# Performance work log

Measured on AMD Instinct MI355X. Metric: run time of the kernel, lower is better.

Reference implementation:

```python
import jax, jax.numpy as jnp
import numpy as np

N_QUBITS = 8
N_LAYERS = 3
DIM = 2 ** N_QUBITS  # 256


def _ry(t):
    # t: scalar or [B] -> [2,2] or [B,2,2] complex64
    c = jnp.cos(t / 2).astype(jnp.complex64)
    s = jnp.sin(t / 2).astype(jnp.complex64)
    return jnp.stack([jnp.stack([c, -s], -1), jnp.stack([s, c], -1)], -2)


def _rz(t):
    e = jnp.exp(-0.5j * t.astype(jnp.complex64))
    z = jnp.zeros_like(e)
    return jnp.stack([jnp.stack([e, z], -1), jnp.stack([z, jnp.conj(e)], -1)], -2)


def _rx(t):
    c = jnp.cos(t / 2).astype(jnp.complex64)
    s = (-1j) * jnp.sin(t / 2).astype(jnp.complex64)
    return jnp.stack([jnp.stack([c, s], -1), jnp.stack([s, c], -1)], -2)


def _apply_1q(state, U, wire):
    # state: [B, 256] complex64; U: [2,2] (shared) or [B,2,2] (per-sample)
    B = state.shape[0]
    l = 2 ** wire
    r = 2 ** (N_QUBITS - wire - 1)
    s = state.reshape(B, l, 2, r)
    if U.ndim == 2:
        s = jnp.einsum('ij,bljr->blir', U, s)
    else:
        s = jnp.einsum('bij,bljr->blir', U, s)
    return s.reshape(B, DIM)


def _apply_cnot(state, c_wire):
    # CNOT with control c_wire, target c_wire+1 (adjacent, as in the circuit)
    B = state.shape[0]
    l = 2 ** c_wire
    r = 2 ** (N_QUBITS - c_wire - 2)
    s = state.reshape(B, l, 2, 2, r)  # [B, left, ctrl, tgt, right]
    s = jnp.stack([s[:, :, 0], s[:, :, 1, ::-1]], axis=2)  # flip target where ctrl=1
    return s.reshape(B, DIM)


def _circuit(x, weights):
    B = x.shape[0]
    state = jnp.zeros((B, DIM), jnp.complex64).at[:, 0].set(1.0)
    # angle encoding: RY(x_i*pi) then RZ(x_i*pi) on each wire (per-sample angles)
    for i in range(N_QUBITS):
        ang = x[:, i] * jnp.pi
        state = _apply_1q(state, _ry(ang), i)
        state = _apply_1q(state, _rz(ang), i)
    # variational layers: RX(w), RY(w) per qubit, then CNOT ladder
    idx = 0
    for _ in range(N_LAYERS):
        for q in range(N_QUBITS):
            state = _apply_1q(state, _rx(weights[idx]), q)
            state = _apply_1q(state, _ry(weights[idx + 1]), q)
            idx += 2
        for q in range(N_QUBITS - 1):
            state = _apply_cnot(state, q)
    # <Z_i> = P(bit_i = 0) - P(bit_i = 1)
    p = (jnp.abs(state) ** 2).reshape((B,) + (2,) * N_QUBITS)
    outs = []
    for i in range(N_QUBITS):
        axes = tuple(j + 1 for j in range(N_QUBITS) if j != i)
        m = p.sum(axes)  # [B, 2]
        outs.append(m[:, 0] - m[:, 1])
    return jnp.stack(outs, -1).astype(jnp.float32)  # [B, 8]


def setup_inputs() -> dict:
    key = jax.random.key(0)
    k1, k2 = jax.random.split(key)
    x = jax.random.normal(k1, (16384, 8), dtype=jnp.float32)
    weights = jax.random.normal(k2, (48,), dtype=jnp.float32) * 0.1
    return {"x": x, "weights": weights}


def reference(x, weights):
    return _circuit(x, weights)
```

## Files before the change

### kernel.cpp

```cpp
#include <hip/hip_runtime.h>
#include <math.h>

#define PI_F 3.14159265358979323846f

typedef _Float16 h16x8 __attribute__((ext_vector_type(8)));
typedef float f32x4 __attribute__((ext_vector_type(4)));
typedef unsigned int u32x4 __attribute__((ext_vector_type(4)));

#define APAGE 4112
#define P2STR 146


__device__ __forceinline__ void gpair(float2& a, const float2 p, const int mb,
                                      const float g0x, const float g0y,
                                      const float g1x, const float g1y) {
    const float e0y = mb ? -g0y : g0y;
    const float f1x = mb ? -g1x : g1x;
    const float nx = g0x * a.x - e0y * a.y + f1x * p.x - g1y * p.y;
    const float ny = g0x * a.y + e0y * a.x + f1x * p.y + g1y * p.x;
    a.x = nx; a.y = ny;
}

__device__ __forceinline__ void apply_g(float2 a[4], const int b, const int lane,
                                        const float g0x, const float g0y,
                                        const float g1x, const float g1y) {
    if (b >= 2) {
        const int lb = b - 2;
        const int mb = (lane >> lb) & 1;
#pragma unroll
        for (int j = 0; j < 4; ++j) {
            float2 p;
            p.x = __shfl_xor(a[j].x, 1 << lb, 64);
            p.y = __shfl_xor(a[j].y, 1 << lb, 64);
            gpair(a[j], p, mb, g0x, g0y, g1x, g1y);
        }
    } else if (b == 1) {
        float2 o0 = a[0], o1 = a[1], o2 = a[2], o3 = a[3];
        gpair(a[0], o2, 0, g0x, g0y, g1x, g1y);
        gpair(a[2], o0, 1, g0x, g0y, g1x, g1y);
        gpair(a[1], o3, 0, g0x, g0y, g1x, g1y);
        gpair(a[3], o1, 1, g0x, g0y, g1x, g1y);
    } else {
        float2 o0 = a[0], o1 = a[1], o2 = a[2], o3 = a[3];
        gpair(a[0], o1, 0, g0x, g0y, g1x, g1y);
        gpair(a[1], o0, 1, g0x, g0y, g1x, g1y);
        gpair(a[2], o3, 0, g0x, g0y, g1x, g1y);
        gpair(a[3], o2, 1, g0x, g0y, g1x, g1y);
    }
}

__device__ __forceinline__ void apply_cnot_g(float2 a[4], const int cw, const int lane) {
    if (cw <= 4) {
        const int lt = (6 - cw) - 2;
        const int lc = lt + 1;
        const bool ctrl = ((lane >> lc) & 1) != 0;
#pragma unroll
        for (int j = 0; j < 4; ++j) {
            float px = __shfl_xor(a[j].x, 1 << lt, 64);
            float py = __shfl_xor(a[j].y, 1 << lt, 64);
            a[j].x = ctrl ? px : a[j].x;
            a[j].y = ctrl ? py : a[j].y;
        }
    } else if (cw == 5) {
        const bool ctrl = (lane & 1) != 0;
        float2 t;
        t = a[0]; a[0].x = ctrl ? a[2].x : a[0].x; a[0].y = ctrl ? a[2].y : a[0].y;
        a[2].x = ctrl ? t.x : a[2].x; a[2].y = ctrl ? t.y : a[2].y;
        t = a[1]; a[1].x = ctrl ? a[3].x : a[1].x; a[1].y = ctrl ? a[3].y : a[1].y;
        a[3].x = ctrl ? t.x : a[3].x; a[3].y = ctrl ? t.y : a[3].y;
    } else {
        float2 t = a[2]; a[2] = a[3]; a[3] = t;
    }
}

__device__ __forceinline__ unsigned int packh2(float lo, float hi) {
    unsigned short l = __builtin_bit_cast(unsigned short, (_Float16)lo);
    unsigned short h = __builtin_bit_cast(unsigned short, (_Float16)hi);
    return ((unsigned int)h << 16) | (unsigned int)l;
}

__device__ __forceinline__ float2 cmulf(float2 a, float2 b) {
    return make_float2(a.x * b.x - a.y * b.y, a.x * b.y + a.y * b.x);
}

__device__ __forceinline__ h16x8 negh8(h16x8 v) {
    u32x4 u = __builtin_bit_cast(u32x4, v);
    u ^= (u32x4){0x80008000u, 0x80008000u, 0x80008000u, 0x80008000u};
    return __builtin_bit_cast(h16x8, u);
}

__global__ __launch_bounds__(64) void ubuild_kernel(const float* __restrict__ w,
                                                    unsigned short* __restrict__ ub16) {
    __shared__ float wc[48];
    __shared__ float wsn[48];
    const int tid = threadIdx.x;
    if (tid < 48) {
        float s, c;
        __sincosf(w[tid] * 0.5f, &s, &c);
        wc[tid] = c; wsn[tid] = s;
    }
    __syncthreads();

    const int lane = tid;
    const int n = blockIdx.x;

    float2 e0q[8], e1q[8];
#pragma unroll
    for (int q = 0; q < 8; ++q) {
        const int k = 2 * q;
        const float c0 = wc[k], s0 = wsn[k];
        const float c1 = wc[k + 1], s1 = wsn[k + 1];
        const float2 g0 = make_float2(c1 * c0, s1 * s0);
        const float2 g1 = make_float2(-s1 * c0, -c1 * s0);
        const int nq = (n >> (7 - q)) & 1;
        e0q[q] = nq ? g1 : g0;
        e1q[q] = nq ? make_float2(g0.x, -g0.y)
                    : make_float2(-g1.x, g1.y);
    }

    float2 a[4];
#pragma unroll
    for (int j = 0; j < 4; ++j) {
        const int m = lane * 4 + j;
        const int v = m ^ (m >> 1);
        float2 acc = ((v >> 7) & 1) ? e1q[0] : e0q[0];
#pragma unroll
        for (int q = 1; q < 8; ++q)
            acc = cmulf(acc, ((v >> (7 - q)) & 1) ? e1q[q] : e0q[q]);
        a[j] = acc;
    }

#pragma unroll
    for (int L = 1; L < 3; ++L) {
#pragma unroll
        for (int q = 0; q < 8; ++q) {
            const int k = 2 * (L * 8 + q);
            const float c0 = wc[k], s0 = wsn[k];
            const float c1 = wc[k + 1], s1 = wsn[k + 1];
            const float g0x = c1 * c0, g0y = s1 * s0;
            const float g1x = -s1 * c0, g1y = -c1 * s0;
            apply_g(a, 7 - q, lane, g0x, g0y, g1x, g1y);
        }
#pragma unroll
        for (int cwire = 0; cwire < 7; ++cwire) apply_cnot_g(a, cwire, lane);
    }

    const int base = (n >> 5) * 8192 + (n & 31);
#pragma unroll
    for (int j = 0; j < 4; ++j) {
        const int m = lane * 4 + j;
        ub16[base + m * 32] =
            __builtin_bit_cast(unsigned short, (_Float16)a[j].x);
        ub16[65536 + base + m * 32] =
            __builtin_bit_cast(unsigned short, (_Float16)a[j].y);
    }
}

__device__ __forceinline__ void loadB4(h16x8 bf[4], const char* ub, const size_t boff[4],
                                       const int kk) {
#pragma unroll
    for (int f = 0; f < 4; ++f)
        bf[f] = *(const h16x8*)(ub + (size_t)kk * 16384 + boff[f]);
}

__device__ __forceinline__ void loadA8(h16x8 ar[4], h16x8 ai[4], const char* apc,
                                       const unsigned int aoff, const int kk) {
#pragma unroll
    for (int rt = 0; rt < 4; ++rt)
        ar[rt] = *(const h16x8*)(apc + kk * APAGE + rt * 1024 + aoff);
#pragma unroll
    for (int rt = 0; rt < 4; ++rt)
        ai[rt] = *(const h16x8*)(apc + 8 * APAGE + kk * APAGE + rt * 1024 + aoff);
}

__device__ __forceinline__ void mfma32(f32x4 aR[4][2], f32x4 aI[4][2],
                                       const h16x8 ar[4], const h16x8 ai[4],
                                       const h16x8 bf[4]) {
#pragma unroll
    for (int rt = 0; rt < 4; ++rt) {
        const h16x8 nai = negh8(ai[rt]);
#pragma unroll
        for (int cf = 0; cf < 2; ++cf) {
            aR[rt][cf] = __builtin_amdgcn_mfma_f32_16x16x32_f16(ar[rt], bf[cf],
                                                                aR[rt][cf], 0, 0, 0);
            aR[rt][cf] = __builtin_amdgcn_mfma_f32_16x16x32_f16(nai, bf[2 + cf],
                                                                aR[rt][cf], 0, 0, 0);
            aI[rt][cf] = __builtin_amdgcn_mfma_f32_16x16x32_f16(ai[rt], bf[cf],
                                                                aI[rt][cf], 0, 0, 0);
            aI[rt][cf] = __builtin_amdgcn_mfma_f32_16x16x32_f16(ar[rt], bf[2 + cf],
                                                                aI[rt][cf], 0, 0, 0);
        }
    }
}

__global__ __launch_bounds__(512, 2) void gemm_kernel(const float* __restrict__ x,
                                                      const unsigned short* __restrict__ upack,
                                                      float* __restrict__ out) {
    __shared__ __align__(16) char smem[64 * P2STR * 8];

    const int tid = threadIdx.x;
    const int lane = tid & 63;
    const int wv = tid >> 6;
    const int c15 = lane & 15;
    const int g = lane >> 4;

    const char* ub = (const char*)upack;
    size_t boff[4];
    {
        const int cb0 = wv * 32;
        boff[0] = (size_t)(cb0 + c15) * 64 + g * 16;
        boff[1] = (size_t)(cb0 + 16 + c15) * 64 + g * 16;
        boff[2] = 131072 + boff[0];
        boff[3] = 131072 + boff[1];
    }
    h16x8 b0[4], b1[4], b2[4], b3[4];
    loadB4(b0, ub, boff, 0);
    loadB4(b1, ub, boff, 1);
    loadB4(b2, ub, boff, 2);
    loadB4(b3, ub, boff, 3);

    {
        const int row = tid >> 3;
        const int t8 = tid & 7;
        const int grow = blockIdx.x * 64 + row;

        const float4* xp = (const float4*)(x + grow * 8);
        float4 xa = xp[0], xb = xp[1];
        float ang[8] = {xa.x, xa.y, xa.z, xa.w, xb.x, xb.y, xb.z, xb.w};

        float2 v0[8], v1[8];
#pragma unroll
        for (int i = 0; i < 8; ++i) {
            float s, c;
            __sincosf(ang[i] * (PI_F * 0.5f), &s, &c);
            v0[i] = make_float2(c * c, -c * s);
            v1[i] = make_float2(s * c, s * s);
        }

        float2 pre = (t8 & 4) ? v1[0] : v0[0];
        pre = cmulf(pre, (t8 & 2) ? v1[1] : v0[1]);
        pre = cmulf(pre, (t8 & 1) ? v1[2] : v0[2]);

        const int swz = (row >> 1) & 3;
        char* reb = smem + t8 * APAGE + row * 64;
        char* imb = smem + (8 + t8) * APAGE + row * 64;

#pragma unroll
        for (int b4 = 0; b4 < 2; ++b4) {
            float2 p3 = cmulf(pre, b4 ? v1[3] : v0[3]);
#pragma unroll
            for (int b3 = 0; b3 < 2; ++b3) {
                float2 p4 = cmulf(p3, b3 ? v1[4] : v0[4]);
                u32x4 qre, qim;
#pragma unroll
                for (int b2 = 0; b2 < 2; ++b2) {
                    float2 p5 = cmulf(p4, b2 ? v1[5] : v0[5]);
#pragma unroll
                    for (int b1 = 0; b1 < 2; ++b1) {
                        float2 p6 = cmulf(p5, b1 ? v1[6] : v0[6]);
                        const float2 amp0 = cmulf(p6, v0[7]);
                        const float2 amp1 = cmulf(p6, v1[7]);
                        const int pos = (b2 << 1) | b1;
                        qre[pos] = packh2(amp0.x, amp1.x);
                        qim[pos] = packh2(amp0.y, amp1.y);
                    }
                }
                const int c = (b4 << 1) | b3;
                *(u32x4*)(reb + ((c ^ swz) * 16)) = qre;
                *(u32x4*)(imb + ((c ^ swz) * 16)) = qim;
            }
        }
    }
    __syncthreads();

    const unsigned int aoff = c15 * 64 + ((g ^ ((c15 >> 1) & 3)) * 16);
    const char* apc = (const char*)smem;

    f32x4 aR[4][2], aI[4][2];
#pragma unroll
    for (int rt = 0; rt < 4; ++rt)
#pragma unroll
        for (int cf = 0; cf < 2; ++cf) {
            f32x4 z = {0.f, 0.f, 0.f, 0.f};
            aR[rt][cf] = z; aI[rt][cf] = z;
        }

    h16x8 ar0[4], ai0[4], ar1[4], ai1[4];
    loadA8(ar0, ai0, apc, aoff, 0);

    loadA8(ar1, ai1, apc, aoff, 1);  mfma32(aR, aI, ar0, ai0, b0);  loadB4(b0, ub, boff, 4);
    loadA8(ar0, ai0, apc, aoff, 2);  mfma32(aR, aI, ar1, ai1, b1);  loadB4(b1, ub, boff, 5);
    loadA8(ar1, ai1, apc, aoff, 3);  mfma32(aR, aI, ar0, ai0, b2);  loadB4(b2, ub, boff, 6);
    loadA8(ar0, ai0, apc, aoff, 4);  mfma32(aR, aI, ar1, ai1, b3);  loadB4(b3, ub, boff, 7);
    loadA8(ar1, ai1, apc, aoff, 5);  mfma32(aR, aI, ar0, ai0, b0);
    loadA8(ar0, ai0, apc, aoff, 6);  mfma32(aR, aI, ar1, ai1, b1);
    loadA8(ar1, ai1, apc, aoff, 7);  mfma32(aR, aI, ar0, ai0, b2);
                                     mfma32(aR, aI, ar1, ai1, b3);

    __syncthreads();

    {
        float2* P2 = (float2*)smem;
#pragma unroll
        for (int rt = 0; rt < 4; ++rt) {
#pragma unroll
            for (int r = 0; r < 4; ++r) {
                const float p0 = aR[rt][0][r] * aR[rt][0][r] + aI[rt][0][r] * aI[rt][0][r];
                const float p1 = aR[rt][1][r] * aR[rt][1][r] + aI[rt][1][r] * aI[rt][1][r];
                const int row = rt * 16 + g * 4 + r;
                P2[row * P2STR + wv * 18 + c15] = make_float2(p0, p1);
            }
        }
    }
    __syncthreads();

    {
        const float2* P2 = (const float2*)smem;
        const int row = tid >> 3;
        const int w2 = tid & 7;

        const float4* base = (const float4*)(P2 + row * P2STR + w2 * 18);
        float S[16], D[16];
#pragma unroll
        for (int k = 0; k < 8; ++k) {
            const float4 q = base[k];
            S[2 * k]     = q.x + q.y;  D[2 * k]     = q.x - q.y;
            S[2 * k + 1] = q.z + q.w;  D[2 * k + 1] = q.z - q.w;
        }
        float s2[8], w1p[8];
#pragma unroll
        for (int k = 0; k < 8; ++k) { s2[k] = S[2*k] + S[2*k+1]; w1p[k] = S[2*k] - S[2*k+1]; }
        float s4[4], w2p[4];
#pragma unroll
        for (int k = 0; k < 4; ++k) { s4[k] = s2[2*k] + s2[2*k+1]; w2p[k] = s2[2*k] - s2[2*k+1]; }
        const float s8a = s4[0] + s4[1], s8b = s4[2] + s4[3];
        const float W0 = s8a + s8b;
        const float W8 = s8a - s8b;
        const float W4 = (s4[0] - s4[1]) + (s4[2] - s4[3]);
        const float W2 = w2p[0] + w2p[1] + w2p[2] + w2p[3];
        float W1 = 0.f, Sd = 0.f;
#pragma unroll
        for (int k = 0; k < 8; ++k) { W1 += w1p[k]; Sd += D[2*k] + D[2*k+1]; }

        float zp[8];
        zp[0] = (w2 & 4) ? -W0 : W0;
        zp[1] = (w2 & 2) ? -W0 : W0;
        zp[2] = (w2 & 1) ? -W0 : W0;
        zp[3] = Sd;
        zp[4] = W8;
        zp[5] = W4;
        zp[6] = W2;
        zp[7] = W1;

#pragma unroll
        for (int i = 0; i < 8; ++i) {
            zp[i] += __shfl_xor(zp[i], 1, 64);
            zp[i] += __shfl_xor(zp[i], 2, 64);
            zp[i] += __shfl_xor(zp[i], 4, 64);
        }

        if (w2 == 0) {
            float* po = out + (size_t)(blockIdx.x * 64 + row) * 8;
            *(float4*)po       = make_float4(zp[0], zp[1], zp[2], zp[3]);
            *(float4*)(po + 4) = make_float4(zp[4], zp[5], zp[6], zp[7]);
        }
    }
}

extern "C" void kernel_launch(void* const* d_in, const int* in_sizes, int n_in,
                              void* d_out, int out_size, void* d_ws, size_t ws_size,
                              hipStream_t stream) {
    const float* x = (const float*)d_in[0];
    const float* w = (const float*)d_in[1];
    float* out = (float*)d_out;
    const int B = in_sizes[0] / 8;

    unsigned short* ub16 = (unsigned short*)d_ws;
    ubuild_kernel<<<256, 64, 0, stream>>>(w, ub16);

    gemm_kernel<<<B / 64, 512, 0, stream>>>(x, (const unsigned short*)d_ws, out);
}
```

Before: 20.49 us.

## Halve rows per block to 32 and raise occupancy target

Each block now processes 32 batch rows instead of 64, using 16 threads per row for state preparation, 2 row tiles per wave in the MFMA loop, and half the shared memory. The grid doubles and launch bounds now ask for 8 blocks per CU, aiming for more parallelism and better latency hiding across the 256 CUs. In exchange, each block reloads the full unitary from global/L2 for half the rows, doubling B-matrix traffic per output row. Half the threads also sit idle in the final reduction.

```diff
diff --git a/kernel.cpp b/kernel.cpp
--- a/kernel.cpp
+++ b/kernel.cpp
@@ -7,9 +7,9 @@
 typedef float f32x4 __attribute__((ext_vector_type(4)));
 typedef unsigned int u32x4 __attribute__((ext_vector_type(4)));
 
-#define APAGE 4112
+#define ROWS 32
+#define APAGE 2064
 #define P2STR 146
-
 
 __device__ __forceinline__ void gpair(float2& a, const float2 p, const int mb,
                                       const float g0x, const float g0y,
@@ -163,21 +163,21 @@
         bf[f] = *(const h16x8*)(ub + (size_t)kk * 16384 + boff[f]);
 }
 
-__device__ __forceinline__ void loadA8(h16x8 ar[4], h16x8 ai[4], const char* apc,
-                                       const unsigned int aoff, const int kk) {
-#pragma unroll
-    for (int rt = 0; rt < 4; ++rt)
+__device__ __forceinline__ void loadA4c(h16x8 ar[2], h16x8 ai[2], const char* apc,
+                                        const unsigned int aoff, const int kk) {
+#pragma unroll
+    for (int rt = 0; rt < 2; ++rt)
         ar[rt] = *(const h16x8*)(apc + kk * APAGE + rt * 1024 + aoff);
 #pragma unroll
-    for (int rt = 0; rt < 4; ++rt)
+    for (int rt = 0; rt < 2; ++rt)
         ai[rt] = *(const h16x8*)(apc + 8 * APAGE + kk * APAGE + rt * 1024 + aoff);
 }
 
-__device__ __forceinline__ void mfma32(f32x4 aR[4][2], f32x4 aI[4][2],
-                                       const h16x8 ar[4], const h16x8 ai[4],
-                                       const h16x8 bf[4]) {
-#pragma unroll
-    for (int rt = 0; rt < 4; ++rt) {
+__device__ __forceinline__ void mfma16c(f32x4 aR[2][2], f32x4 aI[2][2],
+                                        const h16x8 ar[2], const h16x8 ai[2],
+                                        const h16x8 bf[4]) {
+#pragma unroll
+    for (int rt = 0; rt < 2; ++rt) {
         const h16x8 nai = negh8(ai[rt]);
 #pragma unroll
         for (int cf = 0; cf < 2; ++cf) {
@@ -193,10 +193,10 @@
     }
 }
 
-__global__ __launch_bounds__(512, 2) void gemm_kernel(const float* __restrict__ x,
+__global__ __launch_bounds__(512, 8) void gemm_kernel(const float* __restrict__ x,
                                                       const unsigned short* __restrict__ upack,
                                                       float* __restrict__ out) {
-    __shared__ __align__(16) char smem[64 * P2STR * 8];
+    __shared__ __align__(16) char smem[ROWS * P2STR * 8];
 
     const int tid = threadIdx.x;
     const int lane = tid & 63;
@@ -220,9 +220,9 @@
     loadB4(b3, ub, boff, 3);
 
     {
-        const int row = tid >> 3;
-        const int t8 = tid & 7;
-        const int grow = blockIdx.x * 64 + row;
+        const int row = tid >> 4;
+        const int t16 = tid & 15;
+        const int grow = blockIdx.x * ROWS + row;
 
         const float4* xp = (const float4*)(x + grow * 8);
         float4 xa = xp[0], xb = xp[1];
@@ -237,72 +237,76 @@
             v1[i] = make_float2(s * c, s * s);
         }
 
-        float2 pre = (t8 & 4) ? v1[0] : v0[0];
-        pre = cmulf(pre, (t8 & 2) ? v1[1] : v0[1]);
-        pre = cmulf(pre, (t8 & 1) ? v1[2] : v0[2]);
+        float2 pre = (t16 & 8) ? v1[0] : v0[0];
+        pre = cmulf(pre, (t16 & 4) ? v1[1] : v0[1]);
+        pre = cmulf(pre, (t16 & 2) ? v1[2] : v0[2]);
+        pre = cmulf(pre, (t16 & 1) ? v1[3] : v0[3]);
 
         const int swz = (row >> 1) & 3;
-        char* reb = smem + t8 * APAGE + row * 64;
-        char* imb = smem + (8 + t8) * APAGE + row * 64;
-
-#pragma unroll
-        for (int b4 = 0; b4 < 2; ++b4) {
-            float2 p3 = cmulf(pre, b4 ? v1[3] : v0[3]);
-#pragma unroll
-            for (int b3 = 0; b3 < 2; ++b3) {
-                float2 p4 = cmulf(p3, b3 ? v1[4] : v0[4]);
-                u32x4 qre, qim;
-#pragma unroll
-                for (int b2 = 0; b2 < 2; ++b2) {
-                    float2 p5 = cmulf(p4, b2 ? v1[5] : v0[5]);
-#pragma unroll
-                    for (int b1 = 0; b1 < 2; ++b1) {
-                        float2 p6 = cmulf(p5, b1 ? v1[6] : v0[6]);
-                        const float2 amp0 = cmulf(p6, v0[7]);
-                        const float2 amp1 = cmulf(p6, v1[7]);
-                        const int pos = (b2 << 1) | b1;
-                        qre[pos] = packh2(amp0.x, amp1.x);
-                        qim[pos] = packh2(amp0.y, amp1.y);
-                    }
+        const int kk = t16 >> 1;
+        const int half = t16 & 1;
+        char* reb = smem + kk * APAGE + row * 64;
+        char* imb = smem + (8 + kk) * APAGE + row * 64;
+
+        u32x4 qre0, qre1, qim0, qim1;
+#pragma unroll
+        for (int b3 = 0; b3 < 2; ++b3) {
+            float2 p4 = cmulf(pre, b3 ? v1[4] : v0[4]);
+#pragma unroll
+            for (int b2 = 0; b2 < 2; ++b2) {
+                float2 p5 = cmulf(p4, b2 ? v1[5] : v0[5]);
+#pragma unroll
+                for (int b1 = 0; b1 < 2; ++b1) {
+                    float2 p6 = cmulf(p5, b1 ? v1[6] : v0[6]);
+                    const float2 amp0 = cmulf(p6, v0[7]);
+                    const float2 amp1 = cmulf(p6, v1[7]);
+                    const int j = (b3 << 2) | (b2 << 1) | b1;
+                    const unsigned int vre = packh2(amp0.x, amp1.x);
+                    const unsigned int vim = packh2(amp0.y, amp1.y);
+                    if (j < 4) { qre0[j] = vre; qim0[j] = vim; }
+                    else       { qre1[j - 4] = vre; qim1[j - 4] = vim; }
                 }
-                const int c = (b4 << 1) | b3;
-                *(u32x4*)(reb + ((c ^ swz) * 16)) = qre;
-                *(u32x4*)(imb + ((c ^ swz) * 16)) = qim;
-            }
-        }
+            }
+        }
+        const int s0 = (half * 2) ^ swz;
+        const int s1 = (half * 2 + 1) ^ swz;
+        *(u32x4*)(reb + s0 * 16) = qre0;
+        *(u32x4*)(reb + s1 * 16) = qre1;
+        *(u32x4*)(imb + s0 * 16) = qim0;
+        *(u32x4*)(imb + s1 * 16) = qim1;
     }
     __syncthreads();
 
     const unsigned int aoff = c15 * 64 + ((g ^ ((c15 >> 1) & 3)) * 16);
     const char* apc = (const char*)smem;
 
-    f32x4 aR[4][2], aI[4][2];
-#pragma unroll
-    for (int rt = 0; rt < 4; ++rt)
+    f32x4 aR[2][2], aI[2][2];
+#pragma unroll
+    for (int rt = 0; rt < 2; ++rt)
 #pragma unroll
         for (int cf = 0; cf < 2; ++cf) {
             f32x4 z = {0.f, 0.f, 0.f, 0.f};
             aR[rt][cf] = z; aI[rt][cf] = z;
         }
 
-    h16x8 ar0[4], ai0[4], ar1[4], ai1[4];
-    loadA8(ar0, ai0, apc, aoff, 0);
-
-    loadA8(ar1, ai1, apc, aoff, 1);  mfma32(aR, aI, ar0, ai0, b0);  loadB4(b0, ub, boff, 4);
-    loadA8(ar0, ai0, apc, aoff, 2);  mfma32(aR, aI, ar1, ai1, b1);  loadB4(b1, ub, boff, 5);
-    loadA8(ar1, ai1, apc, aoff, 3);  mfma32(aR, aI, ar0, ai0, b2);  loadB4(b2, ub, boff, 6);
-    loadA8(ar0, ai0, apc, aoff, 4);  mfma32(aR, aI, ar1, ai1, b3);  loadB4(b3, ub, boff, 7);
-    loadA8(ar1, ai1, apc, aoff, 5);  mfma32(aR, aI, ar0, ai0, b0);
-    loadA8(ar0, ai0, apc, aoff, 6);  mfma32(aR, aI, ar1, ai1, b1);
-    loadA8(ar1, ai1, apc, aoff, 7);  mfma32(aR, aI, ar0, ai0, b2);
-                                     mfma32(aR, aI, ar1, ai1, b3);
+    h16x8 ar0[2], ai0[2], ar1[2], ai1[2];
+    loadA4c(ar0, ai0, apc, aoff, 0);
+
+    loadA4c(ar1, ai1, apc, aoff, 1);  mfma16c(aR, aI, ar0, ai0, b0);  loadB4(b0, ub, boff, 4);
+    loadA4c(ar0, ai0, apc, aoff, 2);  mfma16c(aR, aI, ar1, ai1, b1);  loadB4(b1, ub, boff, 5);
+    loadA4c(ar1, ai1, apc, aoff, 3);  mfma16c(aR, aI, ar0, ai0, b2);  loadB4(b2, ub, boff, 6);
+    loadA4c(ar0, ai0, apc, aoff, 4);  mfma16c(aR, aI, ar1, ai1, b3);  loadB4(b3, ub, boff, 7);
+    loadA4c(ar1, ai1, apc, aoff, 5);  mfma16c(aR, aI, ar0, ai0, b0);
+    loadA4c(ar0, ai0, apc, aoff, 6);  mfma16c(aR, aI, ar1, ai1, b1);
+    loadA4c(ar1, ai1, apc, aoff, 7);  mfma16c(aR, aI, ar0, ai0, b2);
+                                      mfma16c(aR, aI, ar1, ai1, b3);
 
     __syncthreads();
 
     {
         float2* P2 = (float2*)smem;
 #pragma unroll
-        for (int rt = 0; rt < 4; ++rt) {
+        for (int rt = 0; rt < 2; ++rt) {
 #pragma unroll
             for (int r = 0; r < 4; ++r) {
                 const float p0 = aR[rt][0][r] * aR[rt][0][r] + aI[rt][0][r] * aI[rt][0][r];
@@ -316,53 +320,56 @@
 
     {
         const float2* P2 = (const float2*)smem;
-        const int row = tid >> 3;
-        const int w2 = tid & 7;
-
-        const float4* base = (const float4*)(P2 + row * P2STR + w2 * 18);
-        float S[16], D[16];
-#pragma unroll
-        for (int k = 0; k < 8; ++k) {
-            const float4 q = base[k];
-            S[2 * k]     = q.x + q.y;  D[2 * k]     = q.x - q.y;
-            S[2 * k + 1] = q.z + q.w;  D[2 * k + 1] = q.z - q.w;
-        }
-        float s2[8], w1p[8];
-#pragma unroll
-        for (int k = 0; k < 8; ++k) { s2[k] = S[2*k] + S[2*k+1]; w1p[k] = S[2*k] - S[2*k+1]; }
-        float s4[4], w2p[4];
-#pragma unroll
-        for (int k = 0; k < 4; ++k) { s4[k] = s2[2*k] + s2[2*k+1]; w2p[k] = s2[2*k] - s2[2*k+1]; }
-        const float s8a = s4[0] + s4[1], s8b = s4[2] + s4[3];
-        const float W0 = s8a + s8b;
-        const float W8 = s8a - s8b;
-        const float W4 = (s4[0] - s4[1]) + (s4[2] - s4[3]);
-        const float W2 = w2p[0] + w2p[1] + w2p[2] + w2p[3];
-        float W1 = 0.f, Sd = 0.f;
-#pragma unroll
-        for (int k = 0; k < 8; ++k) { W1 += w1p[k]; Sd += D[2*k] + D[2*k+1]; }
-
-        float zp[8];
-        zp[0] = (w2 & 4) ? -W0 : W0;
-        zp[1] = (w2 & 2) ? -W0 : W0;
-        zp[2] = (w2 & 1) ? -W0 : W0;
-        zp[3] = Sd;
-        zp[4] = W8;
-        zp[5] = W4;
-        zp[6] = W2;
-        zp[7] = W1;
-
-#pragma unroll
-        for (int i = 0; i < 8; ++i) {
-            zp[i] += __shfl_xor(zp[i], 1, 64);
-            zp[i] += __shfl_xor(zp[i], 2, 64);
-            zp[i] += __shfl_xor(zp[i], 4, 64);
-        }
-
-        if (w2 == 0) {
-            float* po = out + (size_t)(blockIdx.x * 64 + row) * 8;
-            *(float4*)po       = make_float4(zp[0], zp[1], zp[2], zp[3]);
-            *(float4*)(po + 4) = make_float4(zp[4], zp[5], zp[6], zp[7]);
+        const int row = tid >> 4;
+        const int sub = tid & 15;
+
+        if (sub < 8) {
+            const int w2 = sub;
+            const float4* base = (const float4*)(P2 + row * P2STR + w2 * 18);
+            float S[16], D[16];
+#pragma unroll
+            for (int k = 0; k < 8; ++k) {
+                const float4 q = base[k];
+                S[2 * k]     = q.x + q.y;  D[2 * k]     = q.x - q.y;
+                S[2 * k + 1] = q.z + q.w;  D[2 * k + 1] = q.z - q.w;
+            }
+            float s2[8], w1p[8];
+#pragma unroll
+            for (int k = 0; k < 8; ++k) { s2[k] = S[2*k] + S[2*k+1]; w1p[k] = S[2*k] - S[2*k+1]; }
+            float s4[4], w2p[4];
+#pragma unroll
+            for (int k = 0; k < 4; ++k) { s4[k] = s2[2*k] + s2[2*k+1]; w2p[k] = s2[2*k] - s2[2*k+1]; }
+            const float s8a = s4[0] + s4[1], s8b = s4[2] + s4[3];
+            const float W0 = s8a + s8b;
+            const float W8 = s8a - s8b;
+            const float W4 = (s4[0] - s4[1]) + (s4[2] - s4[3]);
+            const float W2 = w2p[0] + w2p[1] + w2p[2] + w2p[3];
+            float W1 = 0.f, Sd = 0.f;
+#pragma unroll
+            for (int k = 0; k < 8; ++k) { W1 += w1p[k]; Sd += D[2*k] + D[2*k+1]; }
+
+            float zp[8];
+            zp[0] = (w2 & 4) ? -W0 : W0;
+            zp[1] = (w2 & 2) ? -W0 : W0;
+            zp[2] = (w2 & 1) ? -W0 : W0;
+            zp[3] = Sd;
+            zp[4] = W8;
+            zp[5] = W4;
+            zp[6] = W2;
+            zp[7] = W1;
+
+#pragma unroll
+            for (int i = 0; i < 8; ++i) {
+                zp[i] += __shfl_xor(zp[i], 1, 64);
+                zp[i] += __shfl_xor(zp[i], 2, 64);
+                zp[i] += __shfl_xor(zp[i], 4, 64);
+            }
+
+            if (w2 == 0) {
+                float* po = out + (size_t)(blockIdx.x * ROWS + row) * 8;
+                *(float4*)po       = make_float4(zp[0], zp[1], zp[2], zp[3]);
+                *(float4*)(po + 4) = make_float4(zp[4], zp[5], zp[6], zp[7]);
+            }
         }
     }
 }
@@ -378,5 +385,5 @@
     unsigned short* ub16 = (unsigned short*)d_ws;
     ubuild_kernel<<<256, 64, 0, stream>>>(w, ub16);
 
-    gemm_kernel<<<B / 64, 512, 0, stream>>>(x, (const unsigned short*)d_ws, out);
-}
+    gemm_kernel<<<B / ROWS, 512, 0, stream>>>(x, (const unsigned short*)d_ws, out);
+}
```

Result: slower. 44.27 us (+116.0%).
